# Kernel tuning notes

Measured on AMD Instinct MI355X. Metric: run time of the kernel, lower is better.

## Reference

```python
import jax, jax.numpy as jnp
import numpy as np

SOFT_TAU = 0.5
MAX_TEMP = 40.0
LABEL_SMOOTH = 0.1


def setup_inputs() -> dict:
    key = jax.random.key(0)
    k1, k2 = jax.random.split(key)
    B, Tv, Tw, D = 64, 128, 128, 256
    video_features = jax.random.normal(k1, (B, Tv, D), dtype=jnp.float32)
    wifi_features = jax.random.normal(k2, (B, Tw, D), dtype=jnp.float32)
    logit_scale = jnp.ones((), dtype=jnp.float32)
    return {"video_features": video_features, "wifi_features": wifi_features, "logit_scale": logit_scale}


def _cross_entropy_ls(logits, labels):
    # torch CrossEntropyLoss(label_smoothing=0.1), mean reduction
    logp = jax.nn.log_softmax(logits, axis=-1)
    nll = -jnp.take_along_axis(logp, labels[:, None], axis=1)[:, 0]
    smooth = -jnp.mean(logp, axis=-1)
    return jnp.mean((1.0 - LABEL_SMOOTH) * nll + LABEL_SMOOTH * smooth)


def reference(video_features, wifi_features, logit_scale):
    B = video_features.shape[0]
    # [B, B, Tv, Tw] dense cross-modal similarity
    sim = jnp.einsum('imd,jnd->ijmn', video_features, wifi_features)
    sim_d = jax.lax.stop_gradient(sim)
    # video->wifi soft pooling over Tw
    attn_v2w = jax.nn.softmax(sim_d / SOFT_TAU, axis=3)
    soft_sim_v2w = jnp.sum(sim * attn_v2w, axis=3)  # [B, B, Tv]
    # wifi->video soft pooling over Tv
    attn_w2v = jax.nn.softmax(sim_d / SOFT_TAU, axis=2)
    soft_sim_w2v = jnp.sum(sim * attn_w2v, axis=2)  # [B, B, Tw]
    # frame-level softmax pooling to global similarity
    fw_v = jax.nn.softmax(jax.lax.stop_gradient(soft_sim_v2w) / SOFT_TAU, axis=2)
    sim_v2w_global = jnp.sum(soft_sim_v2w * fw_v, axis=2)  # [B, B]
    fw_w = jax.nn.softmax(jax.lax.stop_gradient(soft_sim_w2v) / SOFT_TAU, axis=2)
    sim_w2v_global = jnp.sum(soft_sim_w2v * fw_w, axis=2)  # [B, B]
    dense_similarity = (sim_v2w_global + sim_w2v_global) / 2.0
    scale = jnp.minimum(logit_scale, MAX_TEMP)
    logits_per_video = scale * dense_similarity
    logits_per_wifi = logits_per_video.T
    labels = jnp.arange(B, dtype=jnp.int32)
    loss_video = _cross_entropy_ls(logits_per_video, labels)
    loss_wifi = _cross_entropy_ls(logits_per_wifi, labels)
    return (loss_video + loss_wifi) / 2.0
```

## Files before the change

### kernel.cpp

```cpp
#include <hip/hip_runtime.h>
#include <hip/hip_bf16.h>

typedef __attribute__((ext_vector_type(8))) short bf16x8;
typedef __attribute__((ext_vector_type(16))) float f32x16;
typedef __attribute__((ext_vector_type(4))) unsigned short u16x4;

#define TT 128
#define DD 256
#define HBUF 32768
#define PARTOFF 65536
#define K2L 2.8853900817779268f

__device__ __forceinline__ unsigned short f2bf(float f) {
  unsigned int x = __float_as_uint(f);
  x += 0x7fffu + ((x >> 16) & 1u);
  return (unsigned short)(x >> 16);
}

__device__ __forceinline__ bf16x8 pack8(float4 lo, float4 hi) {
  bf16x8 v;
  v[0] = (short)f2bf(lo.x); v[1] = (short)f2bf(lo.y);
  v[2] = (short)f2bf(lo.z); v[3] = (short)f2bf(lo.w);
  v[4] = (short)f2bf(hi.x); v[5] = (short)f2bf(hi.y);
  v[6] = (short)f2bf(hi.z); v[7] = (short)f2bf(hi.w);
  return v;
}

__global__ __launch_bounds__(256) void conv_kernel(
    const float* __restrict__ v, const float* __restrict__ w,
    unsigned short* __restrict__ vb, unsigned short* __restrict__ wb) {
  const int idx = blockIdx.x * 256 + threadIdx.x;
  float4 a = reinterpret_cast<const float4*>(v)[idx];
  float4 b = reinterpret_cast<const float4*>(w)[idx];
  u16x4 pa, pb;
  pa[0] = f2bf(a.x); pa[1] = f2bf(a.y); pa[2] = f2bf(a.z); pa[3] = f2bf(a.w);
  pb[0] = f2bf(b.x); pb[1] = f2bf(b.y); pb[2] = f2bf(b.z); pb[3] = f2bf(b.w);
  reinterpret_cast<u16x4*>(vb)[idx] = pa;
  reinterpret_cast<u16x4*>(wb)[idx] = pb;
}

#define FR(BUF, ROW, KSLOT)                                                   \
  (*(const bf16x8*)(lds + (BUF) * HBUF + (ROW) * 256 +                        \
                    ((((KSLOT)) ^ ((ROW) & 15)) << 4)))

template <bool PRE>
__global__ __launch_bounds__(512, 2) void pair_kernel(
    const float* __restrict__ videof, const float* __restrict__ wifif,
    const unsigned short* __restrict__ videob,
    const unsigned short* __restrict__ wifib,
    float* __restrict__ dense) {
  __shared__ __align__(16) char lds[77824];
  const int tid = threadIdx.x;
  const int bid = blockIdx.x;
  const int i  = bid >> 2, jg = bid & 3;
  const int wid = tid >> 6, l = tid & 63;
  const int l31 = l & 31;
  const int khalf = l >> 5;

  const int o  = wid >> 2;
  const int mg = wid & 1;
  const int cg = (wid >> 1) & 1;

  if (tid < 16) dense[i * 64 + jg * 16 + tid] = 0.0f;

  const char* vsrc  = (const char*)videob + (size_t)i * (TT * DD * 2);
  const char* wsrc0 = (const char*)wifib + (size_t)(jg * 16) * (TT * DD * 2);
  const float* vsrcf  = videof + (size_t)i * (TT * DD);
  const float* wsrcf0 = wifif + (size_t)(jg * 16) * (TT * DD);

  const int crow  = l >> 4;
  const int cslot = l & 15;
  const int frow = tid >> 2, fq = tid & 3;

  const int vbase = (o ? cg : mg) * 64;
  const int wbase = (o ? mg : cg) * 64;

#define STAGE_PRE_(SRC, KH, BUF)                                              \
  do {                                                                        \
    _Pragma("unroll") for (int k_ = 0; k_ < 4; ++k_) {                        \
      const int c_ = wid * 4 + k_;                                            \
      const int r_ = c_ * 4 + crow;                                           \
      const char* s_ = (SRC) + r_ * 512 + (KH) * 256 +                        \
                       ((cslot ^ (r_ & 15)) << 4);                            \
      char* d_ = lds + (BUF) * HBUF + c_ * 1024;                              \
      __builtin_amdgcn_global_load_lds((const void*)s_, (void*)d_, 16, 0, 0); \
    }                                                                         \
  } while (0)

#define STAGE_REG_(SRCF, KH, BUF)                                             \
  do {                                                                        \
    _Pragma("unroll") for (int s_ = 0; s_ < 4; ++s_) {                        \
      const int slot_ = fq * 4 + s_;                                          \
      const float* p_ = (SRCF) + frow * DD + (KH) * 128 + slot_ * 8;          \
      float4 x0_ = *(const float4*)(p_);                                      \
      float4 x1_ = *(const float4*)(p_ + 4);                                  \
      *(bf16x8*)(lds + (BUF) * HBUF + frow * 256 +                            \
                 ((slot_ ^ (frow & 15)) << 4)) = pack8(x0_, x1_);             \
    }                                                                         \
  } while (0)

  if constexpr (PRE) STAGE_PRE_(vsrc, 0, 0); else STAGE_REG_(vsrcf, 0, 0);
  __syncthreads();
  if constexpr (PRE) STAGE_PRE_(vsrc, 1, 1); else STAGE_REG_(vsrcf, 1, 1);
  bf16x8 vf[2][16];
#pragma unroll
  for (int g = 0; g < 2; ++g)
#pragma unroll
    for (int ksl = 0; ksl < 8; ++ksl)
      vf[g][ksl] = FR(0, vbase + g * 32 + l31, 2 * ksl + khalf);
  __syncthreads();
  if constexpr (PRE) STAGE_PRE_(wsrc0, 0, 0); else STAGE_REG_(wsrcf0, 0, 0);
#pragma unroll
  for (int g = 0; g < 2; ++g)
#pragma unroll
    for (int ksl = 0; ksl < 8; ++ksl)
      vf[g][8 + ksl] = FR(1, vbase + g * 32 + l31, 2 * ksl + khalf);
  __syncthreads();

  f32x16 acc[2][2];

#define COMPUTE(BUF, KOFF)                                                    \
  do {                                                                        \
    _Pragma("unroll") for (int ksl = 0; ksl < 8; ++ksl) {                     \
      const int kslot_ = 2 * ksl + khalf;                                     \
      bf16x8 w0_ = FR(BUF, wbase + l31, kslot_);                              \
      bf16x8 w1_ = FR(BUF, wbase + 32 + l31, kslot_);                         \
      bf16x8 v0_ = vf[0][(KOFF) + ksl];                                       \
      bf16x8 v1_ = vf[1][(KOFF) + ksl];                                       \
      if (o == 0) {                                                           \
        acc[0][0] = __builtin_amdgcn_mfma_f32_32x32x16_bf16(v0_, w0_, acc[0][0], 0, 0, 0); \
        acc[0][1] = __builtin_amdgcn_mfma_f32_32x32x16_bf16(v0_, w1_, acc[0][1], 0, 0, 0); \
        acc[1][0] = __builtin_amdgcn_mfma_f32_32x32x16_bf16(v1_, w0_, acc[1][0], 0, 0, 0); \
        acc[1][1] = __builtin_amdgcn_mfma_f32_32x32x16_bf16(v1_, w1_, acc[1][1], 0, 0, 0); \
      } else {                                                                \
        acc[0][0] = __builtin_amdgcn_mfma_f32_32x32x16_bf16(w0_, v0_, acc[0][0], 0, 0, 0); \
        acc[0][1] = __builtin_amdgcn_mfma_f32_32x32x16_bf16(w0_, v1_, acc[0][1], 0, 0, 0); \
        acc[1][0] = __builtin_amdgcn_mfma_f32_32x32x16_bf16(w1_, v0_, acc[1][0], 0, 0, 0); \
        acc[1][1] = __builtin_amdgcn_mfma_f32_32x32x16_bf16(w1_, v1_, acc[1][1], 0, 0, 0); \
      }                                                                       \
    }                                                                         \
  } while (0)

#define EPILOGUE(JJ)                                                          \
  do {                                                                        \
    float* P_ = (float*)(lds + PARTOFF + ((JJ) & 1) * 6144);                  \
    _Pragma("unroll") for (int t = 0; t < 2; ++t) {                           \
      float mx = acc[0][t][0];                                                \
      _Pragma("unroll") for (int r = 1; r < 16; ++r) mx = fmaxf(mx, acc[0][t][r]); \
      _Pragma("unroll") for (int r = 0; r < 16; ++r) mx = fmaxf(mx, acc[1][t][r]); \
      const float mxk = mx * K2L;                                             \
      float se = 0.f, sv = 0.f;                                               \
      _Pragma("unroll") for (int mi = 0; mi < 2; ++mi)                        \
        _Pragma("unroll") for (int r = 0; r < 16; ++r) {                      \
          const float v = acc[mi][t][r];                                      \
          const float e = exp2f(fmaf(v, K2L, -mxk));                          \
          se += e; sv = fmaf(e, v, sv);                                       \
        }                                                                     \
      const float om = __shfl_xor(mx, 32);                                    \
      const float os = __shfl_xor(se, 32);                                    \
      const float ov = __shfl_xor(sv, 32);                                    \
      const float M = fmaxf(mx, om);                                          \
      const float f1 = exp2f((mx - M) * K2L);                                 \
      const float f2 = exp2f((om - M) * K2L);                                 \
      se = fmaf(se, f1, os * f2);                                             \
      sv = fmaf(sv, f1, ov * f2);                                             \
      if (l < 32) {                                                           \
        const int idx_ = o * 256 + mg * 128 + cg * 64 + t * 32 + l;           \
        P_[idx_] = M; P_[512 + idx_] = se; P_[1024 + idx_] = sv;              \
      }                                                                       \
    }                                                                         \
  } while (0)

#define REDUCE(JJ)                                                            \
  do {                                                                        \
    const float* P_ = (const float*)(lds + PARTOFF + ((JJ) & 1) * 6144);      \
    const int oo_ = (wid == 0) ? 1 : 0;                                       \
    float a0_, a1_;                                                           \
    {                                                                         \
      const int c_ = oo_ * 256 + l;                                           \
      const float m0 = P_[c_], m1 = P_[c_ + 128];                             \
      const float M = fmaxf(m0, m1);                                          \
      const float f0 = exp2f((m0 - M) * K2L);                                 \
      const float f1 = exp2f((m1 - M) * K2L);                                 \
      a0_ = fmaf(P_[1024 + c_], f0, P_[1024 + c_ + 128] * f1) /               \
            fmaf(P_[512 + c_], f0, P_[512 + c_ + 128] * f1);                  \
    }                                                                         \
    {                                                                         \
      const int c_ = oo_ * 256 + 64 + l;                                      \
      const float m0 = P_[c_], m1 = P_[c_ + 128];                             \
      const float M = fmaxf(m0, m1);                                          \
      const float f0 = exp2f((m0 - M) * K2L);                                 \
      const float f1 = exp2f((m1 - M) * K2L);                                 \
      a1_ = fmaf(P_[1024 + c_], f0, P_[1024 + c_ + 128] * f1) /               \
            fmaf(P_[512 + c_], f0, P_[512 + c_ + 128] * f1);                  \
    }                                                                         \
    float mx_ = fmaxf(a0_, a1_);                                              \
    _Pragma("unroll") for (int s_ = 1; s_ < 64; s_ <<= 1)                     \
      mx_ = fmaxf(mx_, __shfl_xor(mx_, s_));                                  \
    const float e0_ = exp2f((a0_ - mx_) * K2L);                               \
    const float e1_ = exp2f((a1_ - mx_) * K2L);                               \
    float se_ = e0_ + e1_, sev_ = fmaf(e0_, a0_, e1_ * a1_);                  \
    _Pragma("unroll") for (int s_ = 1; s_ < 64; s_ <<= 1) {                   \
      se_ += __shfl_xor(se_, s_); sev_ += __shfl_xor(sev_, s_);               \
    }                                                                         \
    if (l == 0)                                                               \
      atomicAdd(dense + i * 64 + jg * 16 + (JJ), 0.5f * (sev_ / se_));        \
  } while (0)

  for (int jj = 0; jj < 16; ++jj) {
    const char* wsJ1  = wsrc0 + (size_t)jj * (TT * DD * 2);
    const float* wsJ1f = wsrcf0 + (size_t)jj * (TT * DD);
    if constexpr (PRE) STAGE_PRE_(wsJ1, 1, 1); else STAGE_REG_(wsJ1f, 1, 1);
#pragma unroll
    for (int mi = 0; mi < 2; ++mi)
#pragma unroll
      for (int t = 0; t < 2; ++t)
#pragma unroll
        for (int r = 0; r < 16; ++r) acc[mi][t][r] = 0.f;
    COMPUTE(0, 0);
    __syncthreads();
    if (jj < 15) {
      const char* wsJ2  = wsrc0 + (size_t)(jj + 1) * (TT * DD * 2);
      const float* wsJ2f = wsrcf0 + (size_t)(jj + 1) * (TT * DD);
      if constexpr (PRE) STAGE_PRE_(wsJ2, 0, 0); else STAGE_REG_(wsJ2f, 0, 0);
    }
    COMPUTE(1, 8);
    EPILOGUE(jj);
    __syncthreads();
    if (wid < 2) REDUCE(jj);
  }
}

__global__ __launch_bounds__(64) void loss_kernel(
    const float* __restrict__ dense, const float* __restrict__ scalep,
    float* __restrict__ out) {
  const int i = threadIdx.x;
  const float sc = fminf(scalep[0], 40.0f);
  float mxr = -3.4e38f, mxc = -3.4e38f;
  for (int j = 0; j < 64; ++j) {
    mxr = fmaxf(mxr, sc * dense[i * 64 + j]);
    mxc = fmaxf(mxc, sc * dense[j * 64 + i]);
  }
  float ser = 0.f, sec = 0.f, slr = 0.f, slc = 0.f;
  for (int j = 0; j < 64; ++j) {
    float zr = sc * dense[i * 64 + j];
    float zc = sc * dense[j * 64 + i];
    ser += __expf(zr - mxr); sec += __expf(zc - mxc);
    slr += zr;               slc += zc;
  }
  const float lser = mxr + logf(ser);
  const float lsec = mxc + logf(sec);
  const float zd = sc * dense[i * 65];
  float lv = lser - 0.9f * zd - 0.1f * (slr * (1.0f / 64.0f));
  float lw = lsec - 0.9f * zd - 0.1f * (slc * (1.0f / 64.0f));
  float t = 0.5f * (lv + lw);
#pragma unroll
  for (int s = 1; s < 64; s <<= 1) t += __shfl_xor(t, s);
  if (i == 0) out[0] = t * (1.0f / 64.0f);
}

extern "C" void kernel_launch(void* const* d_in, const int* in_sizes, int n_in,
                              void* d_out, int out_size, void* d_ws, size_t ws_size,
                              hipStream_t stream) {
  (void)in_sizes; (void)n_in; (void)out_size;
  const float* video = (const float*)d_in[0];
  const float* wifi  = (const float*)d_in[1];
  const float* scale = (const float*)d_in[2];
  float* dense = (float*)d_ws;
  unsigned short* vb = (unsigned short*)((char*)d_ws + 16384);
  unsigned short* wb = vb + 64 * TT * DD;

  const bool pre = ws_size >= (size_t)16384 + 2u * 64 * TT * DD * 2;
  if (pre) {
    hipLaunchKernelGGL(conv_kernel, dim3(2048), dim3(256), 0, stream,
                       video, wifi, vb, wb);
    hipLaunchKernelGGL((pair_kernel<true>), dim3(256), dim3(512), 0, stream,
                       video, wifi, vb, wb, dense);
  } else {
    hipLaunchKernelGGL((pair_kernel<false>), dim3(256), dim3(512), 0, stream,
                       video, wifi, vb, wb, dense);
  }
  hipLaunchKernelGGL(loss_kernel, dim3(1), dim3(64), 0, stream,
                     dense, scale, (float*)d_out);
}
```

Measured before the change: 108.6 us.

## Split pair work across 512 blocks and keep video tile in LDS instead of registers

Each block now handles 8 wifi samples instead of 16, doubling the grid to 512 blocks. The video tile is kept resident in LDS and read per MFMA step, no longer preloaded into 32 bf16x8 registers per lane. This frees registers and adds parallelism. In exchange LDS use rises to about 140KB per block, which likely allows only one block per CU, and LDS read traffic grows.

```diff
diff --git a/kernel.cpp b/kernel.cpp
--- a/kernel.cpp
+++ b/kernel.cpp
@@ -7,8 +7,12 @@
 
 #define TT 128
 #define DD 256
-#define HBUF 32768
-#define PARTOFF 65536
+#define NJ 8
+#define VID0 0
+#define VID1 32768
+#define WIF0 65536
+#define WIF1 98304
+#define PARTOFF 131072
 #define K2L 2.8853900817779268f
 
 __device__ __forceinline__ unsigned short f2bf(float f) {
@@ -39,8 +43,8 @@
   reinterpret_cast<u16x4*>(wb)[idx] = pb;
 }
 
-#define FR(BUF, ROW, KSLOT)                                                   \
-  (*(const bf16x8*)(lds + (BUF) * HBUF + (ROW) * 256 +                        \
+#define FR(BASE, ROW, KSLOT)                                                  \
+  (*(const bf16x8*)(lds + (BASE) + (ROW) * 256 +                              \
                     ((((KSLOT)) ^ ((ROW) & 15)) << 4)))
 
 template <bool PRE>
@@ -49,10 +53,10 @@
     const unsigned short* __restrict__ videob,
     const unsigned short* __restrict__ wifib,
     float* __restrict__ dense) {
-  __shared__ __align__(16) char lds[77824];
+  __shared__ __align__(16) char lds[143360];
   const int tid = threadIdx.x;
   const int bid = blockIdx.x;
-  const int i  = bid >> 2, jg = bid & 3;
+  const int i  = bid >> 3, jg = bid & 7;
   const int wid = tid >> 6, l = tid & 63;
   const int l31 = l & 31;
   const int khalf = l >> 5;
@@ -61,83 +65,89 @@
   const int mg = wid & 1;
   const int cg = (wid >> 1) & 1;
 
-  if (tid < 16) dense[i * 64 + jg * 16 + tid] = 0.0f;
+  if (tid < NJ) dense[i * 64 + jg * NJ + tid] = 0.0f;
 
   const char* vsrc  = (const char*)videob + (size_t)i * (TT * DD * 2);
-  const char* wsrc0 = (const char*)wifib + (size_t)(jg * 16) * (TT * DD * 2);
+  const char* wsrc0 = (const char*)wifib + (size_t)(jg * NJ) * (TT * DD * 2);
   const float* vsrcf  = videof + (size_t)i * (TT * DD);
-  const float* wsrcf0 = wifif + (size_t)(jg * 16) * (TT * DD);
+  const float* wsrcf0 = wifif + (size_t)(jg * NJ) * (TT * DD);
 
   const int crow  = l >> 4;
   const int cslot = l & 15;
   const int frow = tid >> 2, fq = tid & 3;
 
-  const int vbase = (o ? cg : mg) * 64;
-  const int wbase = (o ? mg : cg) * 64;
-
-#define STAGE_PRE_(SRC, KH, BUF)                                              \
-  do {                                                                        \
+  const int xr0 = mg * 64 + l31, xr1 = mg * 64 + 32 + l31;
+  const int yc0 = cg * 64 + l31, yc1 = cg * 64 + 32 + l31;
+
+#define STAGE_VID_PRE_()                                                      \
+  do {                                                                        \
+    _Pragma("unroll") for (int k_ = 0; k_ < 8; ++k_) {                        \
+      const int q_ = wid * 8 + k_;                                 \
+      const int h_ = q_ >> 5;                                                 \
+      const int c_ = q_ & 31;                                                 \
+      const int r_ = c_ * 4 + crow;                                           \
+      const char* s_ = vsrc + r_ * 512 + h_ * 256 +                           \
+                       ((cslot ^ (r_ & 15)) << 4);                            \
+      char* d_ = lds + h_ * 32768 + c_ * 1024;                                \
+      __builtin_amdgcn_global_load_lds((const void*)s_, (void*)d_, 16, 0, 0); \
+    }                                                                         \
+  } while (0)
+
+#define STAGE_VID_REG_()                                                      \
+  do {                                                                        \
+    _Pragma("unroll") for (int h_ = 0; h_ < 2; ++h_)                          \
+      _Pragma("unroll") for (int s_ = 0; s_ < 4; ++s_) {                      \
+        const int slot_ = fq * 4 + s_;                                        \
+        const float* p_ = vsrcf + frow * DD + h_ * 128 + slot_ * 8;           \
+        float4 x0_ = *(const float4*)(p_);                                    \
+        float4 x1_ = *(const float4*)(p_ + 4);                                \
+        *(bf16x8*)(lds + h_ * 32768 + frow * 256 +                            \
+                   ((slot_ ^ (frow & 15)) << 4)) = pack8(x0_, x1_);           \
+      }                                                                       \
+  } while (0)
+
+#define STAGE_WIF_PRE_(JJ, KH, BUF)                                           \
+  do {                                                                        \
+    const char* ws_ = wsrc0 + (size_t)(JJ) * (TT * DD * 2);                   \
     _Pragma("unroll") for (int k_ = 0; k_ < 4; ++k_) {                        \
-      const int c_ = wid * 4 + k_;                                            \
+      const int c_ = wid * 4 + k_;                                 \
       const int r_ = c_ * 4 + crow;                                           \
-      const char* s_ = (SRC) + r_ * 512 + (KH) * 256 +                        \
+      const char* s_ = ws_ + r_ * 512 + (KH) * 256 +                          \
                        ((cslot ^ (r_ & 15)) << 4);                            \
-      char* d_ = lds + (BUF) * HBUF + c_ * 1024;                              \
+      char* d_ = lds + WIF0 + (BUF) * 32768 + c_ * 1024;                      \
       __builtin_amdgcn_global_load_lds((const void*)s_, (void*)d_, 16, 0, 0); \
     }                                                                         \
   } while (0)
 
-#define STAGE_REG_(SRCF, KH, BUF)                                             \
-  do {                                                                        \
+#define STAGE_WIF_REG_(JJ, KH, BUF)                                           \
+  do {                                                                        \
+    const float* ws_ = wsrcf0 + (size_t)(JJ) * (TT * DD);                     \
     _Pragma("unroll") for (int s_ = 0; s_ < 4; ++s_) {                        \
       const int slot_ = fq * 4 + s_;                                          \
-      const float* p_ = (SRCF) + frow * DD + (KH) * 128 + slot_ * 8;          \
+      const float* p_ = ws_ + frow * DD + (KH) * 128 + slot_ * 8;             \
       float4 x0_ = *(const float4*)(p_);                                      \
       float4 x1_ = *(const float4*)(p_ + 4);                                  \
-      *(bf16x8*)(lds + (BUF) * HBUF + frow * 256 +                            \
+      *(bf16x8*)(lds + WIF0 + (BUF) * 32768 + frow * 256 +                    \
                  ((slot_ ^ (frow & 15)) << 4)) = pack8(x0_, x1_);             \
     }                                                                         \
   } while (0)
 
-  if constexpr (PRE) STAGE_PRE_(vsrc, 0, 0); else STAGE_REG_(vsrcf, 0, 0);
-  __syncthreads();
-  if constexpr (PRE) STAGE_PRE_(vsrc, 1, 1); else STAGE_REG_(vsrcf, 1, 1);
-  bf16x8 vf[2][16];
-#pragma unroll
-  for (int g = 0; g < 2; ++g)
-#pragma unroll
-    for (int ksl = 0; ksl < 8; ++ksl)
-      vf[g][ksl] = FR(0, vbase + g * 32 + l31, 2 * ksl + khalf);
-  __syncthreads();
-  if constexpr (PRE) STAGE_PRE_(wsrc0, 0, 0); else STAGE_REG_(wsrcf0, 0, 0);
-#pragma unroll
-  for (int g = 0; g < 2; ++g)
-#pragma unroll
-    for (int ksl = 0; ksl < 8; ++ksl)
-      vf[g][8 + ksl] = FR(1, vbase + g * 32 + l31, 2 * ksl + khalf);
-  __syncthreads();
-
   f32x16 acc[2][2];
 
-#define COMPUTE(BUF, KOFF)                                                    \
-  do {                                                                        \
+#define COMPUTE_(VB, WB)                                                      \
+  do {                                                                        \
+    const int xb_ = o ? (WB) : (VB);                                          \
+    const int yb_ = o ? (VB) : (WB);                                          \
     _Pragma("unroll") for (int ksl = 0; ksl < 8; ++ksl) {                     \
       const int kslot_ = 2 * ksl + khalf;                                     \
-      bf16x8 w0_ = FR(BUF, wbase + l31, kslot_);                              \
-      bf16x8 w1_ = FR(BUF, wbase + 32 + l31, kslot_);                         \
-      bf16x8 v0_ = vf[0][(KOFF) + ksl];                                       \
-      bf16x8 v1_ = vf[1][(KOFF) + ksl];                                       \
-      if (o == 0) {                                                           \
-        acc[0][0] = __builtin_amdgcn_mfma_f32_32x32x16_bf16(v0_, w0_, acc[0][0], 0, 0, 0); \
-        acc[0][1] = __builtin_amdgcn_mfma_f32_32x32x16_bf16(v0_, w1_, acc[0][1], 0, 0, 0); \
-        acc[1][0] = __builtin_amdgcn_mfma_f32_32x32x16_bf16(v1_, w0_, acc[1][0], 0, 0, 0); \
-        acc[1][1] = __builtin_amdgcn_mfma_f32_32x32x16_bf16(v1_, w1_, acc[1][1], 0, 0, 0); \
-      } else {                                                                \
-        acc[0][0] = __builtin_amdgcn_mfma_f32_32x32x16_bf16(w0_, v0_, acc[0][0], 0, 0, 0); \
-        acc[0][1] = __builtin_amdgcn_mfma_f32_32x32x16_bf16(w0_, v1_, acc[0][1], 0, 0, 0); \
-        acc[1][0] = __builtin_amdgcn_mfma_f32_32x32x16_bf16(w1_, v0_, acc[1][0], 0, 0, 0); \
-        acc[1][1] = __builtin_amdgcn_mfma_f32_32x32x16_bf16(w1_, v1_, acc[1][1], 0, 0, 0); \
-      }                                                                       \
+      bf16x8 x0_ = FR(xb_, xr0, kslot_);                                      \
+      bf16x8 x1_ = FR(xb_, xr1, kslot_);                                      \
+      bf16x8 y0_ = FR(yb_, yc0, kslot_);                                      \
+      bf16x8 y1_ = FR(yb_, yc1, kslot_);                                      \
+      acc[0][0] = __builtin_amdgcn_mfma_f32_32x32x16_bf16(x0_, y0_, acc[0][0], 0, 0, 0); \
+      acc[0][1] = __builtin_amdgcn_mfma_f32_32x32x16_bf16(x0_, y1_, acc[0][1], 0, 0, 0); \
+      acc[1][0] = __builtin_amdgcn_mfma_f32_32x32x16_bf16(x1_, y0_, acc[1][0], 0, 0, 0); \
+      acc[1][1] = __builtin_amdgcn_mfma_f32_32x32x16_bf16(x1_, y1_, acc[1][1], 0, 0, 0); \
     }                                                                         \
   } while (0)
 
@@ -204,27 +214,28 @@
       se_ += __shfl_xor(se_, s_); sev_ += __shfl_xor(sev_, s_);               \
     }                                                                         \
     if (l == 0)                                                               \
-      atomicAdd(dense + i * 64 + jg * 16 + (JJ), 0.5f * (sev_ / se_));        \
-  } while (0)
-
-  for (int jj = 0; jj < 16; ++jj) {
-    const char* wsJ1  = wsrc0 + (size_t)jj * (TT * DD * 2);
-    const float* wsJ1f = wsrcf0 + (size_t)jj * (TT * DD);
-    if constexpr (PRE) STAGE_PRE_(wsJ1, 1, 1); else STAGE_REG_(wsJ1f, 1, 1);
+      atomicAdd(dense + i * 64 + jg * NJ + (JJ), 0.5f * (sev_ / se_));        \
+  } while (0)
+
+  if constexpr (PRE) { STAGE_VID_PRE_(); STAGE_WIF_PRE_(0, 0, 0); }
+  else               { STAGE_VID_REG_(); STAGE_WIF_REG_(0, 0, 0); }
+  __syncthreads();
+
+  for (int jj = 0; jj < NJ; ++jj) {
+    if constexpr (PRE) STAGE_WIF_PRE_(jj, 1, 1); else STAGE_WIF_REG_(jj, 1, 1);
 #pragma unroll
     for (int mi = 0; mi < 2; ++mi)
 #pragma unroll
       for (int t = 0; t < 2; ++t)
 #pragma unroll
         for (int r = 0; r < 16; ++r) acc[mi][t][r] = 0.f;
-    COMPUTE(0, 0);
+    COMPUTE_(VID0, WIF0);
     __syncthreads();
-    if (jj < 15) {
-      const char* wsJ2  = wsrc0 + (size_t)(jj + 1) * (TT * DD * 2);
-      const float* wsJ2f = wsrcf0 + (size_t)(jj + 1) * (TT * DD);
-      if constexpr (PRE) STAGE_PRE_(wsJ2, 0, 0); else STAGE_REG_(wsJ2f, 0, 0);
+    if (jj < NJ - 1) {
+      if constexpr (PRE) STAGE_WIF_PRE_(jj + 1, 0, 0);
+      else STAGE_WIF_REG_(jj + 1, 0, 0);
     }
-    COMPUTE(1, 8);
+    COMPUTE_(VID1, WIF1);
     EPILOGUE(jj);
     __syncthreads();
     if (wid < 2) REDUCE(jj);
@@ -274,10 +285,10 @@
   if (pre) {
     hipLaunchKernelGGL(conv_kernel, dim3(2048), dim3(256), 0, stream,
                        video, wifi, vb, wb);
-    hipLaunchKernelGGL((pair_kernel<true>), dim3(256), dim3(512), 0, stream,
+    hipLaunchKernelGGL((pair_kernel<true>), dim3(512), dim3(512), 0, stream,
                        video, wifi, vb, wb, dense);
   } else {
-    hipLaunchKernelGGL((pair_kernel<false>), dim3(256), dim3(512), 0, stream,
+    hipLaunchKernelGGL((pair_kernel<false>), dim3(512), dim3(512), 0, stream,
                        video, wifi, vb, wb, dense);
   }
   hipLaunchKernelGGL(loss_kernel, dim3(1), dim3(64), 0, stream,
```

Measured after the change: 111.3 us. 1.02x slower.
